# Performance work log

Hardware: AMD Instinct MI355X
Metric: run time of the kernel (lower is better)

The kernel has to match this reference:

```python
import jax, jax.numpy as jnp
import numpy as np

B, L, D = 128, 512, 768   # batch, bert tokens, bert hidden
J = 32                    # clause boundaries -> S = J + 1 segments
S = J + 1
DM, DF = 200, 200         # transformer d_model / ffn dim
EPS = 1e-5


def _ln(x, g, b):
    m = x.mean(-1, keepdims=True)
    v = ((x - m) ** 2).mean(-1, keepdims=True)
    return (x - m) / jnp.sqrt(v + EPS) * g + b


def setup_inputs() -> dict:
    key = jax.random.key(0)
    ks = jax.random.split(key, 12)
    sc = 0.02
    hidden_state = jax.random.normal(ks[0], (B, L, D), jnp.float32)
    # strictly increasing, positive clause boundaries < L (non-empty segments)
    seg = L // S  # stride ~= 15 tokens per clause
    jitter = jax.random.randint(ks[1], (B, J), 0, seg).astype(jnp.int32)
    clause_idx = jnp.arange(1, J + 1, dtype=jnp.int32)[None, :] * seg + jitter
    p = lambda k, shp: sc * jax.random.normal(k, shp, jnp.float32)
    z = lambda n: jnp.zeros((n,), jnp.float32)
    return {
        'hidden_state': hidden_state,
        'clause_idx': clause_idx,
        'fc5_w': p(ks[2], (1, D)), 'fc5_b': z(1),
        'fc1_w': p(ks[3], (DM, D)), 'fc1_b': z(DM),
        'attn_in_w': p(ks[4], (3 * DM, DM)), 'attn_in_b': z(3 * DM),
        'attn_out_w': p(ks[5], (DM, DM)), 'attn_out_b': z(DM),
        'ln1_g': jnp.ones((DM,), jnp.float32), 'ln1_b': z(DM),
        'lin1_w': p(ks[6], (DF, DM)), 'lin1_b': z(DF),
        'lin2_w': p(ks[7], (DM, DF)), 'lin2_b': z(DM),
        'ln2_g': jnp.ones((DM,), jnp.float32), 'ln2_b': z(DM),
        'fc_w': p(ks[8], (2, 2 * DM)), 'fc_b': z(2),
    }


def reference(hidden_state, clause_idx, fc5_w, fc5_b, fc1_w, fc1_b,
              attn_in_w, attn_in_b, attn_out_w, attn_out_b,
              ln1_g, ln1_b, lin1_w, lin1_b, lin2_w, lin2_b,
              ln2_g, ln2_b, fc_w, fc_b):
    # ---- ragged per-segment attention pooling (batched_index_select) ----
    t = jnp.arange(L)
    # segment id of each token: number of boundaries <= t  -> [B, L] in [0, S)
    seg_id = jnp.sum(t[None, None, :] >= clause_idx[:, :, None], axis=1)
    scores = jnp.einsum('bld,d->bl', hidden_state, fc5_w[0]) + fc5_b[0]  # fc5
    mask = seg_id[:, None, :] == jnp.arange(S)[None, :, None]            # [B,S,L]
    logits = jnp.where(mask, scores[:, None, :], -jnp.inf)
    w = jax.nn.softmax(logits, axis=-1)        # per-segment softmax over tokens
    pooled = jnp.einsum('bsl,bld->bsd', w, hidden_state)                 # [B,S,D]

    # ---- fc1 + TransformerEncoderLayer (post-norm, 1 head, relu, no dropout)
    x = pooled @ fc1_w.T + fc1_b                                         # [B,S,DM]
    qkv = x @ attn_in_w.T + attn_in_b
    q, k, v = jnp.split(qkv, 3, axis=-1)
    a = jax.nn.softmax(jnp.einsum('bqd,bkd->bqk', q, k) * (1.0 / np.sqrt(DM).item()), axis=-1)
    att = jnp.einsum('bqk,bkd->bqd', a, v) @ attn_out_w.T + attn_out_b
    x = _ln(x + att, ln1_g, ln1_b)
    ff = jax.nn.relu(x @ lin1_w.T + lin1_b) @ lin2_w.T + lin2_b
    x = _ln(x + ff, ln2_g, ln2_b)

    # ---- cat(first-token broadcast, rest) then classifier fc ----
    h = jnp.concatenate([jnp.broadcast_to(x[:, :1, :], (B, S - 1, DM)), x[:, 1:, :]], axis=-1)
    return h @ fc_w.T + fc_b                                             # [B, S-1, 2]
```

## Files before the change

kernel.cpp:

```cpp
#include <hip/hip_runtime.h>

#define NB 128
#define LL 512
#define DD 768
#define JJ 32
#define SS 33
#define DM 200

typedef __attribute__((ext_vector_type(8))) short bf8_t;
typedef __attribute__((ext_vector_type(4))) float f4_t;

#define SB_XF   0
#define SB_QB   61440
#define SB_KB   82944
#define SB_VT   104448
#define SB_BLK  131072

static __device__ __forceinline__ unsigned short f2bf(float f) {
  unsigned u = __float_as_uint(f);
  return (unsigned short)((u + 0x7FFFu + ((u >> 16) & 1u)) >> 16);
}

template<int KS>
static __device__ __forceinline__ f4_t mfma_tile(
    const unsigned short* pa, const unsigned short* pw)
{
  f4_t acc = {0.f, 0.f, 0.f, 0.f};
  bf8_t a = *(const bf8_t*)pa;
  bf8_t w = *(const bf8_t*)pw;
#pragma unroll
  for (int s = 1; s < KS; ++s) {
    bf8_t a2 = *(const bf8_t*)(pa + 32 * s);
    bf8_t w2 = *(const bf8_t*)(pw + 32 * s);
    acc = __builtin_amdgcn_mfma_f32_16x16x32_bf16(a, w, acc, 0, 0, 0);
    a = a2; w = w2;
  }
  acc = __builtin_amdgcn_mfma_f32_16x16x32_bf16(a, w, acc, 0, 0, 0);
  return acc;
}

template<int KS>
static __device__ __forceinline__ f4_t mfma_tile_lds(
    const unsigned short* pa, const unsigned short* pw)
{
  f4_t acc = {0.f, 0.f, 0.f, 0.f};
#pragma unroll
  for (int s = 0; s < KS; ++s) {
    bf8_t a = *(const bf8_t*)(pa + 32 * s);
    bf8_t w = *(const bf8_t*)(pw + 32 * s);
    acc = __builtin_amdgcn_mfma_f32_16x16x32_bf16(a, w, acc, 0, 0, 0);
  }
  return acc;
}

__global__ __launch_bounds__(512, 4) void pc_kernel(
    const float* __restrict__ hidden, const int* __restrict__ clause,
    const float* __restrict__ fc5w, unsigned short* __restrict__ pooled_bf,
    const float* __restrict__ fc1_w, const float* __restrict__ ain_w,
    const float* __restrict__ aout_w, const float* __restrict__ lin1_w,
    const float* __restrict__ lin2_w,
    unsigned short* __restrict__ fc1_wb, unsigned short* __restrict__ ain_wb,
    unsigned short* __restrict__ aout_wb, unsigned short* __restrict__ lin1_wb,
    unsigned short* __restrict__ lin2_wb, char* __restrict__ scratch)
{
  const int tid = threadIdx.x;
  if (blockIdx.x >= NB * SS) {
    int t = (blockIdx.x - NB * SS) * 512 + tid;
    if (t < 208 * 768) {
      int n = t / 768, k = t - n * 768;
      fc1_wb[t] = f2bf((n < 200) ? fc1_w[n * 768 + k] : 0.f);
      return;
    }
    t -= 208 * 768;
    if (t < 608 * 224) {
      int n = t / 224, k = t - n * 224;
      ain_wb[t] = f2bf((n < 600 && k < 200) ? ain_w[n * 200 + k] : 0.f);
      return;
    }
    t -= 608 * 224;
    if (t < 208 * 224) {
      int n = t / 224, k = t - n * 224;
      aout_wb[t] = f2bf((n < 200 && k < 200) ? aout_w[n * 200 + k] : 0.f);
      return;
    }
    t -= 208 * 224;
    if (t < 208 * 224) {
      int n = t / 224, k = t - n * 224;
      lin1_wb[t] = f2bf((n < 200 && k < 200) ? lin1_w[n * 200 + k] : 0.f);
      return;
    }
    t -= 208 * 224;
    if (t < 208 * 224) {
      int n = t / 224, k = t - n * 224;
      lin2_wb[t] = f2bf((n < 200 && k < 200) ? lin2_w[n * 200 + k] : 0.f);
      return;
    }
    t -= 208 * 224;
    if (t < NB * 1344) {
      int b = t / 1344, r = t - b * 1344;
      char* sb = scratch + (size_t)b * SB_BLK;
      const uint4 z = make_uint4(0, 0, 0, 0);
      if (r < 384) {
        int bi = r / 192, rr = r - bi * 192;
        int row = rr >> 2, c = rr & 3;
        int off = (bi == 0) ? SB_QB : SB_KB;
        *(uint4*)((unsigned short*)(sb + off) + row * 224 + 192 + c * 8) = z;
      } else {
        int rr = r - 384;
        int row = rr >> 2, c = rr & 3;
        if (row < 208)
          *(uint4*)((unsigned short*)(sb + SB_VT) + row * 64 + 32 + c * 8) = z;
      }
    }
    return;
  }

  int blk = blockIdx.x;
  int b = blk / SS;
  int s = blk - b * SS;
  int t0 = (s == 0) ? 0 : clause[b * JJ + s - 1];
  int t1 = (s == JJ) ? LL : clause[b * JJ + s];
  int nt = t1 - t0;
  if (nt > 64) nt = 64;
  if (nt < 1) nt = 1;

  __shared__ float wsm[64];
  __shared__ __align__(16) float pw[8][772];
  int wave = tid >> 6, lane = tid & 63;

  const float4* w4 = (const float4*)fc5w;
  float4 wa = w4[lane], wwb = w4[lane + 64], wc = w4[lane + 128];

  float4 hv[4][3];
#pragma unroll
  for (int i = 0; i < 4; ++i) {
    int r = wave + 8 * i;
    if (r < nt) {
      const float4* hp = (const float4*)(hidden + ((long long)b * LL + t0 + r) * DD);
      hv[i][0] = hp[lane]; hv[i][1] = hp[lane + 64]; hv[i][2] = hp[lane + 128];
    }
  }
#pragma unroll
  for (int i = 0; i < 4; ++i) {
    int r = wave + 8 * i;
    if (r < nt) {
      float4 h0 = hv[i][0], h1 = hv[i][1], h2 = hv[i][2];
      float acc = h0.x*wa.x + h0.y*wa.y + h0.z*wa.z + h0.w*wa.w
                + h1.x*wwb.x + h1.y*wwb.y + h1.z*wwb.z + h1.w*wwb.w
                + h2.x*wc.x + h2.y*wc.y + h2.z*wc.z + h2.w*wc.w;
#pragma unroll
      for (int off = 32; off; off >>= 1) acc += __shfl_xor(acc, off);
      if (lane == 0) wsm[r] = acc;
    }
  }
  for (int r = wave + 32; r < nt; r += 8) {
    const float4* hp = (const float4*)(hidden + ((long long)b * LL + t0 + r) * DD);
    float4 h0 = hp[lane], h1 = hp[lane + 64], h2 = hp[lane + 128];
    float acc = h0.x*wa.x + h0.y*wa.y + h0.z*wa.z + h0.w*wa.w
              + h1.x*wwb.x + h1.y*wwb.y + h1.z*wwb.z + h1.w*wwb.w
              + h2.x*wc.x + h2.y*wc.y + h2.z*wc.z + h2.w*wc.w;
#pragma unroll
    for (int off = 32; off; off >>= 1) acc += __shfl_xor(acc, off);
    if (lane == 0) wsm[r] = acc;
  }
  __syncthreads();

  if (wave == 0) {
    float v = (lane < nt) ? wsm[lane] : -__builtin_inff();
    float mx = v;
#pragma unroll
    for (int off = 32; off; off >>= 1) mx = fmaxf(mx, __shfl_xor(mx, off));
    float e = (lane < nt) ? __expf(v - mx) : 0.f;
    float sm = e;
#pragma unroll
    for (int off = 32; off; off >>= 1) sm += __shfl_xor(sm, off);
    if (lane < nt) wsm[lane] = e / sm;
  }
  __syncthreads();

  float4 p0 = {0,0,0,0}, p1 = {0,0,0,0}, p2 = {0,0,0,0};
#pragma unroll
  for (int i = 0; i < 4; ++i) {
    int r = wave + 8 * i;
    if (r < nt) {
      float w = wsm[r];
      p0.x = fmaf(w, hv[i][0].x, p0.x); p0.y = fmaf(w, hv[i][0].y, p0.y);
      p0.z = fmaf(w, hv[i][0].z, p0.z); p0.w = fmaf(w, hv[i][0].w, p0.w);
      p1.x = fmaf(w, hv[i][1].x, p1.x); p1.y = fmaf(w, hv[i][1].y, p1.y);
      p1.z = fmaf(w, hv[i][1].z, p1.z); p1.w = fmaf(w, hv[i][1].w, p1.w);
      p2.x = fmaf(w, hv[i][2].x, p2.x); p2.y = fmaf(w, hv[i][2].y, p2.y);
      p2.z = fmaf(w, hv[i][2].z, p2.z); p2.w = fmaf(w, hv[i][2].w, p2.w);
    }
  }
  for (int r = wave + 32; r < nt; r += 8) {
    const float4* hp = (const float4*)(hidden + ((long long)b * LL + t0 + r) * DD);
    float w = wsm[r];
    float4 h0 = hp[lane], h1 = hp[lane + 64], h2 = hp[lane + 128];
    p0.x = fmaf(w, h0.x, p0.x); p0.y = fmaf(w, h0.y, p0.y);
    p0.z = fmaf(w, h0.z, p0.z); p0.w = fmaf(w, h0.w, p0.w);
    p1.x = fmaf(w, h1.x, p1.x); p1.y = fmaf(w, h1.y, p1.y);
    p1.z = fmaf(w, h1.z, p1.z); p1.w = fmaf(w, h1.w, p1.w);
    p2.x = fmaf(w, h2.x, p2.x); p2.y = fmaf(w, h2.y, p2.y);
    p2.z = fmaf(w, h2.z, p2.z); p2.w = fmaf(w, h2.w, p2.w);
  }
  {
    float4* pp = (float4*)&pw[wave][0];
    pp[lane] = p0; pp[lane + 64] = p1; pp[lane + 128] = p2;
  }
  __syncthreads();

  if (tid < 384) {
    float2 acc = make_float2(0.f, 0.f);
#pragma unroll
    for (int w = 0; w < 8; ++w) {
      float2 v = *(const float2*)&pw[w][tid * 2];
      acc.x += v.x; acc.y += v.y;
    }
    ushort2 o;
    o.x = f2bf(acc.x); o.y = f2bf(acc.y);
    *(ushort2*)(pooled_bf + (long long)blk * DD + tid * 2) = o;
  }
}

__global__ __launch_bounds__(512, 4) void k_fc1qkv(
    const unsigned short* __restrict__ pooled,
    const unsigned short* __restrict__ fc1_wb, const float* __restrict__ fc1_b,
    const unsigned short* __restrict__ ain_wb, const float* __restrict__ ain_b,
    char* __restrict__ scratch, float* __restrict__ out)
{
  const int b = blockIdx.x / 3, mt = blockIdx.x % 3, m0 = mt * 16;
  const int tid = threadIdx.x, wv = tid >> 6, lane = tid & 63;
  const int col = lane & 15, quad = lane >> 4, koff = quad * 8;

  if (blockIdx.x < 16) out[blockIdx.x * 512 + tid] = 0.f;

  char* sb = scratch + (size_t)b * SB_BLK;
  float* x_f32 = (float*)(sb + SB_XF);
  unsigned short* q_bf  = (unsigned short*)(sb + SB_QB);
  unsigned short* k_bf  = (unsigned short*)(sb + SB_KB);
  unsigned short* vt_bf = (unsigned short*)(sb + SB_VT);

  __shared__ __align__(16) unsigned short sA[16][776];
  __shared__ __align__(16) unsigned short xb[16][232];

  {
    int r = tid >> 5, c = tid & 31;
    int src = m0 + r; if (src > 32) src = 32;
    const unsigned* gp = (const unsigned*)(pooled + (size_t)(b * SS + src) * DD);
    unsigned* lp = (unsigned*)&sA[r][0];
#pragma unroll
    for (int i = 0; i < 12; ++i) lp[c + 32 * i] = gp[c + 32 * i];
  }
  for (int u = tid; u < 16 * 16; u += 512) {
    int row = u >> 4, c = u & 15;
    ((unsigned*)&xb[row][200])[c] = 0u;
  }
  __syncthreads();

  for (int t = wv; t < 13; t += 8) {
    int n0 = t * 16;
    f4_t acc = mfma_tile_lds<24>(&sA[0][0] + col * 776 + koff,
                                 fc1_wb + (size_t)(n0 + col) * DD + koff);
    int gn = n0 + col;
    if (gn < DM) {
      float bv = fc1_b[gn];
#pragma unroll
      for (int r = 0; r < 4; ++r) {
        int row = quad * 4 + r;
        float v = acc[r] + bv;
        x_f32[(m0 + row) * 208 + gn] = v;
        xb[row][gn] = f2bf(v);
      }
    }
  }
  __syncthreads();

  for (int t = wv; t < 38; t += 8) {
    int n0 = t * 16;
    f4_t acc = mfma_tile_lds<7>(&xb[0][0] + col * 232 + koff,
                                ain_wb + (size_t)(n0 + col) * 224 + koff);
    int gn = n0 + col;
    if (gn < 600) {
      float bv = ain_b[gn];
#pragma unroll
      for (int r = 0; r < 4; ++r) {
        int gm = m0 + quad * 4 + r;
        unsigned short bfv = f2bf(acc[r] + bv);
        if (gn < 200)      q_bf[gm * 224 + gn] = bfv;
        else if (gn < 400) k_bf[gm * 224 + (gn - 200)] = bfv;
        else if (gm < SS)  vt_bf[(gn - 400) * 64 + gm] = bfv;
      }
    }
  }
}

__global__ __launch_bounds__(512, 4) void k_postattn(
    const unsigned short* __restrict__ aout_wb, const float* __restrict__ aout_b,
    const float* __restrict__ ln1_g, const float* __restrict__ ln1_b,
    const unsigned short* __restrict__ lin1_wb, const float* __restrict__ lin1_b,
    const unsigned short* __restrict__ lin2_wb, const float* __restrict__ lin2_b,
    const float* __restrict__ ln2_g, const float* __restrict__ ln2_b,
    const float* __restrict__ fcw, const float* __restrict__ fcb,
    char* __restrict__ scratch, float* __restrict__ out)
{
  const int b = blockIdx.x / 3, mt = blockIdx.x % 3, m0 = mt * 16;
  const int tid = threadIdx.x, wv = tid >> 6, lane = tid & 63;
  const int col = lane & 15, quad = lane >> 4, koff = quad * 8;

  char* sb = scratch + (size_t)b * SB_BLK;
  const unsigned short* q_bf  = (const unsigned short*)(sb + SB_QB);
  const unsigned short* k_bf  = (const unsigned short*)(sb + SB_KB);
  const unsigned short* vt_bf = (const unsigned short*)(sb + SB_VT);
  const float* x_f32 = (const float*)(sb + SB_XF);

  __shared__ float tc[16][211];
  __shared__ __align__(16) unsigned short Pb[16][72];
  __shared__ __align__(16) unsigned short yb[16][232];
  __shared__ __align__(16) unsigned short fb[16][232];
  for (int u = tid; u < 16 * 16; u += 512) {
    int row = u >> 4, c = u & 15;
    ((unsigned*)&yb[row][200])[c] = 0u;
    ((unsigned*)&fb[row][200])[c] = 0u;
  }

  for (int t = wv; t < 3; t += 8) {
    int n0 = t * 16;
    f4_t acc = mfma_tile<7>(q_bf + (m0 + col) * 224 + koff,
                            k_bf + (n0 + col) * 224 + koff);
    int gn = n0 + col;
#pragma unroll
    for (int r = 0; r < 4; ++r)
      tc[quad * 4 + r][gn] = acc[r] * 0.07071067811865475f;
  }
  __syncthreads();

  for (int r = wv; r < 16; r += 8) {
    bool live = (m0 + r) < SS;
    float v = (lane < SS && live) ? tc[r][lane] : -__builtin_inff();
    float mx = v;
#pragma unroll
    for (int off = 32; off; off >>= 1) mx = fmaxf(mx, __shfl_xor(mx, off));
    float e = (lane < SS && live) ? __expf(v - mx) : 0.f;
    float sm = e;
#pragma unroll
    for (int off = 32; off; off >>= 1) sm += __shfl_xor(sm, off);
    Pb[r][lane] = (lane < SS && live) ? f2bf(e / sm) : (unsigned short)0;
  }
  __syncthreads();

  for (int t = wv; t < 13; t += 8) {
    int n0 = t * 16;
    f4_t acc = mfma_tile_lds<2>(&Pb[0][0] + col * 72 + koff,
                                vt_bf + (n0 + col) * 64 + koff);
    int gn = n0 + col;
    if (gn < DM) {
#pragma unroll
      for (int r = 0; r < 4; ++r)
        fb[quad * 4 + r][gn] = f2bf(acc[r]);
    }
  }
  __syncthreads();

  for (int t = wv; t < 13; t += 8) {
    int n0 = t * 16;
    f4_t acc = mfma_tile_lds<7>(&fb[0][0] + col * 232 + koff,
                                aout_wb + (size_t)(n0 + col) * 224 + koff);
    int gn = n0 + col;
    float bv = (gn < DM) ? aout_b[gn] : 0.f;
#pragma unroll
    for (int r = 0; r < 4; ++r) {
      int row = quad * 4 + r;
      float v = acc[r] + bv;
      if (gn < DM) v += x_f32[(m0 + row) * 208 + gn];
      tc[row][gn] = v;
    }
  }
  __syncthreads();

  for (int r = wv; r < 16; r += 8) {
    float* p = &tc[r][0];
    float vals[4]; float s = 0.f;
#pragma unroll
    for (int i = 0; i < 4; ++i) { int k = lane + 64 * i; vals[i] = (k < DM) ? p[k] : 0.f; s += vals[i]; }
#pragma unroll
    for (int off = 32; off; off >>= 1) s += __shfl_xor(s, off);
    float mean = s * (1.f / DM);
    float vs = 0.f;
#pragma unroll
    for (int i = 0; i < 4; ++i) { int k = lane + 64 * i; if (k < DM) { float d = vals[i] - mean; vs += d * d; } }
#pragma unroll
    for (int off = 32; off; off >>= 1) vs += __shfl_xor(vs, off);
    float rstd = rsqrtf(vs * (1.f / DM) + 1e-5f);
#pragma unroll
    for (int i = 0; i < 4; ++i) {
      int k = lane + 64 * i;
      if (k < DM) {
        float o = (vals[i] - mean) * rstd * ln1_g[k] + ln1_b[k];
        p[k] = o;
        yb[r][k] = f2bf(o);
      }
    }
  }
  __syncthreads();

  for (int t = wv; t < 13; t += 8) {
    int n0 = t * 16;
    f4_t acc = mfma_tile_lds<7>(&yb[0][0] + col * 232 + koff,
                                lin1_wb + (size_t)(n0 + col) * 224 + koff);
    int gn = n0 + col;
    if (gn < DM) {
      float bv = lin1_b[gn];
#pragma unroll
      for (int r = 0; r < 4; ++r)
        fb[quad * 4 + r][gn] = f2bf(fmaxf(acc[r] + bv, 0.f));
    }
  }
  __syncthreads();

  for (int t = wv; t < 13; t += 8) {
    int n0 = t * 16;
    f4_t acc = mfma_tile_lds<7>(&fb[0][0] + col * 232 + koff,
                                lin2_wb + (size_t)(n0 + col) * 224 + koff);
    int gn = n0 + col;
    if (gn < DM) {
      float bv = lin2_b[gn];
#pragma unroll
      for (int r = 0; r < 4; ++r) {
        int row = quad * 4 + r;
        tc[row][gn] = acc[r] + bv + tc[row][gn];
      }
    }
  }
  __syncthreads();

  for (int r = wv; r < 16; r += 8) {
    float* p = &tc[r][0];
    float vals[4]; float s = 0.f;
#pragma unroll
    for (int i = 0; i < 4; ++i) { int k = lane + 64 * i; vals[i] = (k < DM) ? p[k] : 0.f; s += vals[i]; }
#pragma unroll
    for (int off = 32; off; off >>= 1) s += __shfl_xor(s, off);
    float mean = s * (1.f / DM);
    float vs = 0.f;
#pragma unroll
    for (int i = 0; i < 4; ++i) { int k = lane + 64 * i; if (k < DM) { float d = vals[i] - mean; vs += d * d; } }
#pragma unroll
    for (int off = 32; off; off >>= 1) vs += __shfl_xor(vs, off);
    float rstd = rsqrtf(vs * (1.f / DM) + 1e-5f);
#pragma unroll
    for (int i = 0; i < 4; ++i) {
      int k = lane + 64 * i;
      if (k < DM) p[k] = (vals[i] - mean) * rstd * ln2_g[k] + ln2_b[k];
    }
  }
  __syncthreads();

  for (int r = wv; r < 16; r += 8) {
    int grow = m0 + r;
    if (grow >= SS) continue;
    const float* p = &tc[r][0];
    if (grow == 0) {
      float s0 = 0.f, s1 = 0.f;
#pragma unroll
      for (int i = 0; i < 4; ++i) {
        int k = lane + 64 * i;
        if (k < DM) { float v = p[k]; s0 += v * fcw[k]; s1 += v * fcw[400 + k]; }
      }
#pragma unroll
      for (int off = 32; off; off >>= 1) {
        s0 += __shfl_xor(s0, off);
        s1 += __shfl_xor(s1, off);
      }
      if (lane < 32) {
        atomicAdd(&out[(b * 32 + lane) * 2 + 0], s0 + fcb[0]);
        atomicAdd(&out[(b * 32 + lane) * 2 + 1], s1 + fcb[1]);
      }
    } else {
      int j = grow - 1;
      float a0 = 0.f, a1 = 0.f;
#pragma unroll
      for (int i = 0; i < 4; ++i) {
        int k = lane + 64 * i;
        if (k < DM) { float v = p[k]; a0 += v * fcw[200 + k]; a1 += v * fcw[600 + k]; }
      }
#pragma unroll
      for (int off = 32; off; off >>= 1) {
        a0 += __shfl_xor(a0, off);
        a1 += __shfl_xor(a1, off);
      }
      if (lane == 0) {
        atomicAdd(&out[(b * 32 + j) * 2 + 0], a0);
        atomicAdd(&out[(b * 32 + j) * 2 + 1], a1);
      }
    }
  }
}

extern "C" void kernel_launch(void* const* d_in, const int* in_sizes, int n_in,
                              void* d_out, int out_size, void* d_ws, size_t ws_size,
                              hipStream_t stream)
{
  (void)in_sizes; (void)n_in; (void)out_size; (void)ws_size;
  const float* hidden = (const float*)d_in[0];
  const int*   clause = (const int*)d_in[1];
  const float* fc5_w  = (const float*)d_in[2];
  const float* fc1_w  = (const float*)d_in[4];
  const float* fc1_b  = (const float*)d_in[5];
  const float* ain_w  = (const float*)d_in[6];
  const float* ain_b  = (const float*)d_in[7];
  const float* aout_w = (const float*)d_in[8];
  const float* aout_b = (const float*)d_in[9];
  const float* ln1_g  = (const float*)d_in[10];
  const float* ln1_b  = (const float*)d_in[11];
  const float* lin1_w = (const float*)d_in[12];
  const float* lin1_b = (const float*)d_in[13];
  const float* lin2_w = (const float*)d_in[14];
  const float* lin2_b = (const float*)d_in[15];
  const float* ln2_g  = (const float*)d_in[16];
  const float* ln2_b  = (const float*)d_in[17];
  const float* fc_w   = (const float*)d_in[18];
  const float* fc_b   = (const float*)d_in[19];
  float* out = (float*)d_out;

  char* w8 = (char*)d_ws;
  unsigned short* pooled_bf = (unsigned short*)(w8 + 0);
  char* scratch = w8 + 6520832;
  size_t wbase = 6520832 + (size_t)NB * SB_BLK;
  unsigned short* fc1_wb  = (unsigned short*)(w8 + wbase);
  unsigned short* ain_wb  = (unsigned short*)(w8 + wbase + 319488);
  unsigned short* aout_wb = (unsigned short*)(w8 + wbase + 591872);
  unsigned short* lin1_wb = (unsigned short*)(w8 + wbase + 685056);
  unsigned short* lin2_wb = (unsigned short*)(w8 + wbase + 778240);

  pc_kernel<<<dim3(NB * SS + 1187), 512, 0, stream>>>(
      hidden, clause, fc5_w, pooled_bf,
      fc1_w, ain_w, aout_w, lin1_w, lin2_w,
      fc1_wb, ain_wb, aout_wb, lin1_wb, lin2_wb, scratch);
  k_fc1qkv<<<dim3(NB * 3), 512, 0, stream>>>(pooled_bf, fc1_wb, fc1_b,
      ain_wb, ain_b, scratch, out);
  k_postattn<<<dim3(NB * 3), 512, 0, stream>>>(aout_wb, aout_b, ln1_g, ln1_b,
      lin1_wb, lin1_b, lin2_wb, lin2_b, ln2_g, ln2_b, fc_w, fc_b,
      scratch, out);
}
```

Before: 360.9 us.

## Fuse fc1/QKV and post-attention kernels with per-batch atomic barrier

Merges the fc1+QKV kernel and the post-attention kernel into one launch. The three row-tile blocks of each batch now synchronise through a global atomic counter with spin-wait instead of a kernel boundary, and one shared-memory buffer is reused across the two phases. Zeroing of the output and the counters moves into the spare blocks of the first kernel. This removes one launch and its tail gap, at the cost of relying on all three blocks of a batch being co-resident (384 blocks should fit) and the spin-wait overhead.

```diff
diff --git a/kernel.cpp b/kernel.cpp
--- a/kernel.cpp
+++ b/kernel.cpp
@@ -61,7 +61,8 @@
     const float* __restrict__ lin2_w,
     unsigned short* __restrict__ fc1_wb, unsigned short* __restrict__ ain_wb,
     unsigned short* __restrict__ aout_wb, unsigned short* __restrict__ lin1_wb,
-    unsigned short* __restrict__ lin2_wb, char* __restrict__ scratch)
+    unsigned short* __restrict__ lin2_wb, char* __restrict__ scratch,
+    float* __restrict__ out, int* __restrict__ pcnt)
 {
   const int tid = threadIdx.x;
   if (blockIdx.x >= NB * SS) {
@@ -111,7 +112,12 @@
         if (row < 208)
           *(uint4*)((unsigned short*)(sb + SB_VT) + row * 64 + 32 + c * 8) = z;
       }
-    }
+      return;
+    }
+    t -= NB * 1344;
+    if (t < NB * 32 * 2) { out[t] = 0.f; return; }
+    t -= NB * 32 * 2;
+    if (t < NB) pcnt[t] = 0;
     return;
   }
 
@@ -222,17 +228,21 @@
   }
 }
 
-__global__ __launch_bounds__(512, 4) void k_fc1qkv(
+__global__ __launch_bounds__(512, 4) void k_tx(
     const unsigned short* __restrict__ pooled,
     const unsigned short* __restrict__ fc1_wb, const float* __restrict__ fc1_b,
     const unsigned short* __restrict__ ain_wb, const float* __restrict__ ain_b,
-    char* __restrict__ scratch, float* __restrict__ out)
+    const unsigned short* __restrict__ aout_wb, const float* __restrict__ aout_b,
+    const float* __restrict__ ln1_g, const float* __restrict__ ln1_b,
+    const unsigned short* __restrict__ lin1_wb, const float* __restrict__ lin1_b,
+    const unsigned short* __restrict__ lin2_wb, const float* __restrict__ lin2_b,
+    const float* __restrict__ ln2_g, const float* __restrict__ ln2_b,
+    const float* __restrict__ fcw, const float* __restrict__ fcb,
+    char* __restrict__ scratch, int* __restrict__ pcnt, float* __restrict__ out)
 {
   const int b = blockIdx.x / 3, mt = blockIdx.x % 3, m0 = mt * 16;
   const int tid = threadIdx.x, wv = tid >> 6, lane = tid & 63;
   const int col = lane & 15, quad = lane >> 4, koff = quad * 8;
-
-  if (blockIdx.x < 16) out[blockIdx.x * 512 + tid] = 0.f;
 
   char* sb = scratch + (size_t)b * SB_BLK;
   float* x_f32 = (float*)(sb + SB_XF);
@@ -240,26 +250,31 @@
   unsigned short* k_bf  = (unsigned short*)(sb + SB_KB);
   unsigned short* vt_bf = (unsigned short*)(sb + SB_VT);
 
-  __shared__ __align__(16) unsigned short sA[16][776];
-  __shared__ __align__(16) unsigned short xb[16][232];
+  __shared__ __align__(16) char smem[32256];
+  unsigned short* sA = (unsigned short*)smem;
+  unsigned short* xb = (unsigned short*)(smem + 24832);
+  float*          tc = (float*)smem;
+  unsigned short* Pb = (unsigned short*)(smem + 13504);
+  unsigned short* yb = (unsigned short*)(smem + 15808);
+  unsigned short* fb = (unsigned short*)(smem + 23232);
 
   {
     int r = tid >> 5, c = tid & 31;
     int src = m0 + r; if (src > 32) src = 32;
     const unsigned* gp = (const unsigned*)(pooled + (size_t)(b * SS + src) * DD);
-    unsigned* lp = (unsigned*)&sA[r][0];
+    unsigned* lp = (unsigned*)(sA + r * 776);
 #pragma unroll
     for (int i = 0; i < 12; ++i) lp[c + 32 * i] = gp[c + 32 * i];
   }
   for (int u = tid; u < 16 * 16; u += 512) {
     int row = u >> 4, c = u & 15;
-    ((unsigned*)&xb[row][200])[c] = 0u;
+    ((unsigned*)(xb + row * 232 + 200))[c] = 0u;
   }
   __syncthreads();
 
   for (int t = wv; t < 13; t += 8) {
     int n0 = t * 16;
-    f4_t acc = mfma_tile_lds<24>(&sA[0][0] + col * 776 + koff,
+    f4_t acc = mfma_tile_lds<24>(sA + col * 776 + koff,
                                  fc1_wb + (size_t)(n0 + col) * DD + koff);
     int gn = n0 + col;
     if (gn < DM) {
@@ -269,7 +284,7 @@
         int row = quad * 4 + r;
         float v = acc[r] + bv;
         x_f32[(m0 + row) * 208 + gn] = v;
-        xb[row][gn] = f2bf(v);
+        xb[row * 232 + gn] = f2bf(v);
       }
     }
   }
@@ -277,7 +292,7 @@
 
   for (int t = wv; t < 38; t += 8) {
     int n0 = t * 16;
-    f4_t acc = mfma_tile_lds<7>(&xb[0][0] + col * 232 + koff,
+    f4_t acc = mfma_tile_lds<7>(xb + col * 232 + koff,
                                 ain_wb + (size_t)(n0 + col) * 224 + koff);
     int gn = n0 + col;
     if (gn < 600) {
@@ -292,35 +307,21 @@
       }
     }
   }
-}
-
-__global__ __launch_bounds__(512, 4) void k_postattn(
-    const unsigned short* __restrict__ aout_wb, const float* __restrict__ aout_b,
-    const float* __restrict__ ln1_g, const float* __restrict__ ln1_b,
-    const unsigned short* __restrict__ lin1_wb, const float* __restrict__ lin1_b,
-    const unsigned short* __restrict__ lin2_wb, const float* __restrict__ lin2_b,
-    const float* __restrict__ ln2_g, const float* __restrict__ ln2_b,
-    const float* __restrict__ fcw, const float* __restrict__ fcb,
-    char* __restrict__ scratch, float* __restrict__ out)
-{
-  const int b = blockIdx.x / 3, mt = blockIdx.x % 3, m0 = mt * 16;
-  const int tid = threadIdx.x, wv = tid >> 6, lane = tid & 63;
-  const int col = lane & 15, quad = lane >> 4, koff = quad * 8;
-
-  char* sb = scratch + (size_t)b * SB_BLK;
-  const unsigned short* q_bf  = (const unsigned short*)(sb + SB_QB);
-  const unsigned short* k_bf  = (const unsigned short*)(sb + SB_KB);
-  const unsigned short* vt_bf = (const unsigned short*)(sb + SB_VT);
-  const float* x_f32 = (const float*)(sb + SB_XF);
-
-  __shared__ float tc[16][211];
-  __shared__ __align__(16) unsigned short Pb[16][72];
-  __shared__ __align__(16) unsigned short yb[16][232];
-  __shared__ __align__(16) unsigned short fb[16][232];
+  __syncthreads();
+
+  if (tid == 0) {
+    __threadfence();
+    __hip_atomic_fetch_add(pcnt + b, 1, __ATOMIC_ACQ_REL, __HIP_MEMORY_SCOPE_AGENT);
+    while (__hip_atomic_load(pcnt + b, __ATOMIC_ACQUIRE, __HIP_MEMORY_SCOPE_AGENT) < 3)
+      __builtin_amdgcn_s_sleep(2);
+    __threadfence();
+  }
+  __syncthreads();
+
   for (int u = tid; u < 16 * 16; u += 512) {
     int row = u >> 4, c = u & 15;
-    ((unsigned*)&yb[row][200])[c] = 0u;
-    ((unsigned*)&fb[row][200])[c] = 0u;
+    ((unsigned*)(yb + row * 232 + 200))[c] = 0u;
+    ((unsigned*)(fb + row * 232 + 200))[c] = 0u;
   }
 
   for (int t = wv; t < 3; t += 8) {
@@ -330,13 +331,13 @@
     int gn = n0 + col;
 #pragma unroll
     for (int r = 0; r < 4; ++r)
-      tc[quad * 4 + r][gn] = acc[r] * 0.07071067811865475f;
+      tc[(quad * 4 + r) * 211 + gn] = acc[r] * 0.07071067811865475f;
   }
   __syncthreads();
 
   for (int r = wv; r < 16; r += 8) {
     bool live = (m0 + r) < SS;
-    float v = (lane < SS && live) ? tc[r][lane] : -__builtin_inff();
+    float v = (lane < SS && live) ? tc[r * 211 + lane] : -__builtin_inff();
     float mx = v;
 #pragma unroll
     for (int off = 32; off; off >>= 1) mx = fmaxf(mx, __shfl_xor(mx, off));
@@ -344,26 +345,26 @@
     float sm = e;
 #pragma unroll
     for (int off = 32; off; off >>= 1) sm += __shfl_xor(sm, off);
-    Pb[r][lane] = (lane < SS && live) ? f2bf(e / sm) : (unsigned short)0;
+    Pb[r * 72 + lane] = (lane < SS && live) ? f2bf(e / sm) : (unsigned short)0;
   }
   __syncthreads();
 
   for (int t = wv; t < 13; t += 8) {
     int n0 = t * 16;
-    f4_t acc = mfma_tile_lds<2>(&Pb[0][0] + col * 72 + koff,
+    f4_t acc = mfma_tile_lds<2>(Pb + col * 72 + koff,
                                 vt_bf + (n0 + col) * 64 + koff);
     int gn = n0 + col;
     if (gn < DM) {
 #pragma unroll
       for (int r = 0; r < 4; ++r)
-        fb[quad * 4 + r][gn] = f2bf(acc[r]);
+        fb[(quad * 4 + r) * 232 + gn] = f2bf(acc[r]);
     }
   }
   __syncthreads();
 
   for (int t = wv; t < 13; t += 8) {
     int n0 = t * 16;
-    f4_t acc = mfma_tile_lds<7>(&fb[0][0] + col * 232 + koff,
+    f4_t acc = mfma_tile_lds<7>(fb + col * 232 + koff,
                                 aout_wb + (size_t)(n0 + col) * 224 + koff);
     int gn = n0 + col;
     float bv = (gn < DM) ? aout_b[gn] : 0.f;
@@ -372,13 +373,13 @@
       int row = quad * 4 + r;
       float v = acc[r] + bv;
       if (gn < DM) v += x_f32[(m0 + row) * 208 + gn];
-      tc[row][gn] = v;
+      tc[row * 211 + gn] = v;
     }
   }
   __syncthreads();
 
   for (int r = wv; r < 16; r += 8) {
-    float* p = &tc[r][0];
+    float* p = tc + r * 211;
     float vals[4]; float s = 0.f;
 #pragma unroll
     for (int i = 0; i < 4; ++i) { int k = lane + 64 * i; vals[i] = (k < DM) ? p[k] : 0.f; s += vals[i]; }
@@ -397,7 +398,7 @@
       if (k < DM) {
         float o = (vals[i] - mean) * rstd * ln1_g[k] + ln1_b[k];
         p[k] = o;
-        yb[r][k] = f2bf(o);
+        yb[r * 232 + k] = f2bf(o);
       }
     }
   }
@@ -405,21 +406,21 @@
 
   for (int t = wv; t < 13; t += 8) {
     int n0 = t * 16;
-    f4_t acc = mfma_tile_lds<7>(&yb[0][0] + col * 232 + koff,
+    f4_t acc = mfma_tile_lds<7>(yb + col * 232 + koff,
                                 lin1_wb + (size_t)(n0 + col) * 224 + koff);
     int gn = n0 + col;
     if (gn < DM) {
       float bv = lin1_b[gn];
 #pragma unroll
       for (int r = 0; r < 4; ++r)
-        fb[quad * 4 + r][gn] = f2bf(fmaxf(acc[r] + bv, 0.f));
+        fb[(quad * 4 + r) * 232 + gn] = f2bf(fmaxf(acc[r] + bv, 0.f));
     }
   }
   __syncthreads();
 
   for (int t = wv; t < 13; t += 8) {
     int n0 = t * 16;
-    f4_t acc = mfma_tile_lds<7>(&fb[0][0] + col * 232 + koff,
+    f4_t acc = mfma_tile_lds<7>(fb + col * 232 + koff,
                                 lin2_wb + (size_t)(n0 + col) * 224 + koff);
     int gn = n0 + col;
     if (gn < DM) {
@@ -427,14 +428,14 @@
 #pragma unroll
       for (int r = 0; r < 4; ++r) {
         int row = quad * 4 + r;
-        tc[row][gn] = acc[r] + bv + tc[row][gn];
+        tc[row * 211 + gn] = acc[r] + bv + tc[row * 211 + gn];
       }
     }
   }
   __syncthreads();
 
   for (int r = wv; r < 16; r += 8) {
-    float* p = &tc[r][0];
+    float* p = tc + r * 211;
     float vals[4]; float s = 0.f;
 #pragma unroll
     for (int i = 0; i < 4; ++i) { int k = lane + 64 * i; vals[i] = (k < DM) ? p[k] : 0.f; s += vals[i]; }
@@ -458,7 +459,7 @@
   for (int r = wv; r < 16; r += 8) {
     int grow = m0 + r;
     if (grow >= SS) continue;
-    const float* p = &tc[r][0];
+    const float* p = tc + r * 211;
     if (grow == 0) {
       float s0 = 0.f, s1 = 0.f;
 #pragma unroll
@@ -531,14 +532,14 @@
   unsigned short* aout_wb = (unsigned short*)(w8 + wbase + 591872);
   unsigned short* lin1_wb = (unsigned short*)(w8 + wbase + 685056);
   unsigned short* lin2_wb = (unsigned short*)(w8 + wbase + 778240);
-
-  pc_kernel<<<dim3(NB * SS + 1187), 512, 0, stream>>>(
+  int*            pcnt    = (int*)(w8 + wbase + 871424);
+
+  pc_kernel<<<dim3(NB * SS + 1204), 512, 0, stream>>>(
       hidden, clause, fc5_w, pooled_bf,
       fc1_w, ain_w, aout_w, lin1_w, lin2_w,
-      fc1_wb, ain_wb, aout_wb, lin1_wb, lin2_wb, scratch);
-  k_fc1qkv<<<dim3(NB * 3), 512, 0, stream>>>(pooled_bf, fc1_wb, fc1_b,
-      ain_wb, ain_b, scratch, out);
-  k_postattn<<<dim3(NB * 3), 512, 0, stream>>>(aout_wb, aout_b, ln1_g, ln1_b,
+      fc1_wb, ain_wb, aout_wb, lin1_wb, lin2_wb, scratch, out, pcnt);
+  k_tx<<<dim3(NB * 3), 512, 0, stream>>>(pooled_bf, fc1_wb, fc1_b,
+      ain_wb, ain_b, aout_wb, aout_b, ln1_g, ln1_b,
       lin1_wb, lin1_b, lin2_wb, lin2_b, ln2_g, ln2_b, fc_w, fc_b,
-      scratch, out);
+      scratch, pcnt, out);
 }
```

Result: slower. 408.0 us (+13.0%).
